# Optimization experiments

Hardware: AMD Instinct MI355X
Metric: run time of the kernel (lower is better)

The kernel has to match this reference:

```python
import jax, jax.numpy as jnp
import numpy as np

F = 16      # frames
NV = 4096   # visual points per frame
NT = 512    # tactile points per frame
M = 4096    # model points
SCALE = 0.1


def setup_inputs() -> dict:
    key = jax.random.key(0)
    ks = jax.random.split(key, 6)
    return {
        "state": jax.random.normal(ks[0], (6,), dtype=jnp.float32) * 0.1,
        "model_points": jax.random.normal(ks[1], (M, 3), dtype=jnp.float32),
        "visual_points": jax.random.normal(ks[2], (F, NV, 3), dtype=jnp.float32),
        "tactile_points": jax.random.normal(ks[3], (F, NT, 3), dtype=jnp.float32),
        "physics_pred_states": jax.random.normal(ks[4], (F, 12), dtype=jnp.float32) * 0.1,
        "delta_time": jax.random.uniform(ks[5], (F,), dtype=jnp.float32, minval=0.01, maxval=0.05),
    }


def _skew(a):
    z = jnp.zeros((), a.dtype)
    return jnp.array([[z, -a[2], a[1]],
                      [a[2], z, -a[0]],
                      [-a[1], a[0], z]])


def _rot_from_omega(omega, dt):
    # Rodrigues: R = I + sin(theta*dt) S + (1 - cos(theta*dt)) S@S, S = skew(omega/|omega|)
    theta = jnp.linalg.norm(omega)
    ax = omega / jnp.clip(theta, 1e-8)
    S = _skew(ax)
    return jnp.eye(3, dtype=omega.dtype) + jnp.sin(theta * dt) * S + (1.0 - jnp.cos(theta * dt)) * (S @ S)


def _chamfer(pred, gt):
    # rows: pred [N,3], cols: gt [M,3]; row-min of squared distances, then mean
    d = (jnp.sum(pred * pred, axis=1)[:, None]
         + jnp.sum(gt * gt, axis=1)[None, :]
         - 2.0 * pred @ gt.T)
    return jnp.mean(jnp.min(d, axis=1))


def reference(state, model_points, visual_points, tactile_points, physics_pred_states, delta_time):
    t0 = state[:3]
    r0 = _rot_from_omega(state[3:], jnp.float32(1.0))  # Euler2Mat modeled as axis-angle

    def pose_step(carry, x):
        t, r = carry
        v, omega, dt = x
        t = t + v * dt
        r = _rot_from_omega(omega, dt) @ r
        return (t, r), (t, r)

    _, (ts, rs) = jax.lax.scan(
        pose_step, (t0, r0),
        (physics_pred_states[1:, 6:9], physics_pred_states[1:, 9:12], delta_time[1:]))
    ts = jnp.concatenate([t0[None], ts], axis=0)  # [F,3]
    rs = jnp.concatenate([r0[None], rs], axis=0)  # [F,3,3]

    def frame_loss(acc, x):
        t, r, vp, tp = x
        vc = ((vp - t) @ r) / SCALE
        tc = ((tp - t) @ r) / SCALE
        acc = acc + _chamfer(vc, model_points) + 0.1 * _chamfer(tc, model_points)
        return acc, None

    E_cd, _ = jax.lax.scan(frame_loss, jnp.zeros((), jnp.float32),
                           (ts, rs, visual_points, tactile_points))
    return E_cd
```

## Files before the change

### kernel.cpp

```cpp
#include <hip/hip_runtime.h>
#include <math.h>

#define F_    16
#define NV_   4096
#define NT_   512
#define M_    4096
#define PPF_  (NV_ + NT_)
#define NPTS_ (F_ * PPF_)
#define SCALE_INV 10.0f

#define TPB    256
#define PPT    8
#define PPB    (TPB * PPT)
#define NPB    (NPTS_ / PPB)
#define CHUNK  128
#define NCHUNK (M_ / CHUNK)

__device__ inline void rot_from_omega(float ox, float oy, float oz, float dt,
                                      float* R) {
    float theta = sqrtf(ox * ox + oy * oy + oz * oz);
    float inv = 1.0f / fmaxf(theta, 1e-8f);
    float ax = ox * inv, ay = oy * inv, az = oz * inv;
    float s = sinf(theta * dt);
    float c = 1.0f - cosf(theta * dt);
    R[0] = 1.0f - c * (ay * ay + az * az);
    R[1] = -s * az + c * ax * ay;
    R[2] =  s * ay + c * ax * az;
    R[3] =  s * az + c * ax * ay;
    R[4] = 1.0f - c * (ax * ax + az * az);
    R[5] = -s * ax + c * ay * az;
    R[6] = -s * ax * 0.0f + c * 0.0f;
    R[6] = -s * ay + c * ax * az;
    R[7] =  s * ax + c * ay * az;
    R[8] = 1.0f - c * (ax * ax + ay * ay);
}

__global__ void pose_kernel(const float* __restrict__ state,
                            const float* __restrict__ phys,
                            const float* __restrict__ dts,
                            float* __restrict__ poses,
                            float* __restrict__ out) {
    __shared__ float sRs[F_ * 9];
    __shared__ float sdt[F_ * 3];
    int f = threadIdx.x;
    if (f == 0) out[0] = 0.0f;
    if (f >= 1 && f < F_) {
        float Rs[9];
        float dt = dts[f];
        rot_from_omega(phys[f * 12 + 9], phys[f * 12 + 10], phys[f * 12 + 11], dt, Rs);
        for (int j = 0; j < 9; ++j) sRs[f * 9 + j] = Rs[j];
        sdt[f * 3 + 0] = phys[f * 12 + 6] * dt;
        sdt[f * 3 + 1] = phys[f * 12 + 7] * dt;
        sdt[f * 3 + 2] = phys[f * 12 + 8] * dt;
    }
    __syncthreads();
    if (f == 0) {
        float t[3] = {state[0], state[1], state[2]};
        float R[9];
        rot_from_omega(state[3], state[4], state[5], 1.0f, R);
        for (int i = 0; i < F_; ++i) {
            if (i > 0) {
                t[0] += sdt[i * 3 + 0];
                t[1] += sdt[i * 3 + 1];
                t[2] += sdt[i * 3 + 2];
                float Rn[9];
                const float* Rs = sRs + i * 9;
                for (int r = 0; r < 3; ++r)
                    for (int c2 = 0; c2 < 3; ++c2)
                        Rn[r * 3 + c2] = Rs[r * 3 + 0] * R[0 + c2] +
                                         Rs[r * 3 + 1] * R[3 + c2] +
                                         Rs[r * 3 + 2] * R[6 + c2];
                for (int j = 0; j < 9; ++j) R[j] = Rn[j];
            }
            float* o = poses + i * 12;
            o[0] = t[0]; o[1] = t[1]; o[2] = t[2];
            for (int j = 0; j < 9; ++j) o[3 + j] = R[j] * SCALE_INV;
        }
    }
}

__global__ __launch_bounds__(TPB) void chamfer_main(
    const float* __restrict__ model, const float* __restrict__ vis,
    const float* __restrict__ tac, const float* __restrict__ poses,
    float* __restrict__ partials) {
    __shared__ float4 sfeat[CHUNK];
    __shared__ float sposes[F_ * 12];
    const int pb = blockIdx.x;
    const int ch = blockIdx.y;
    const int mbase = ch * CHUNK;

    if (threadIdx.x < F_ * 12) sposes[threadIdx.x] = poses[threadIdx.x];

    if (threadIdx.x < CHUNK) {
        int i = threadIdx.x;
        float gx = model[(mbase + i) * 3 + 0];
        float gy = model[(mbase + i) * 3 + 1];
        float gz = model[(mbase + i) * 3 + 2];
        sfeat[i] = make_float4(-2.0f * gx, -2.0f * gy, -2.0f * gz,
                               gx * gx + gy * gy + gz * gz);
    }
    __syncthreads();

    float c0[PPT], c1[PPT], c2[PPT], cn[PPT], dm[PPT];
#pragma unroll
    for (int k = 0; k < PPT; ++k) {
        int pt = pb * PPB + k * TPB + threadIdx.x;
        int f = pt / PPF_;
        int loc = pt - f * PPF_;
        const float* p = (loc < NV_) ? (vis + ((size_t)f * NV_ + loc) * 3)
                                     : (tac + ((size_t)f * NT_ + (loc - NV_)) * 3);
        float px = p[0], py = p[1], pz = p[2];
        const float* ps = sposes + f * 12;
        float d0 = px - ps[0], d1 = py - ps[1], d2 = pz - ps[2];
        const float* R = ps + 3;
        float x = d0 * R[0] + d1 * R[3] + d2 * R[6];
        float y = d0 * R[1] + d1 * R[4] + d2 * R[7];
        float z = d0 * R[2] + d1 * R[5] + d2 * R[8];
        c0[k] = x; c1[k] = y; c2[k] = z;
        cn[k] = x * x + y * y + z * z;
        dm[k] = 3.4e38f;
    }

#pragma unroll 4
    for (int m = 0; m < CHUNK; m += 2) {
        float4 ga = sfeat[m];
        float4 gb = sfeat[m + 1];
#pragma unroll
        for (int k = 0; k < PPT; ++k) {
            float da = fmaf(ga.x, c0[k], fmaf(ga.y, c1[k], fmaf(ga.z, c2[k], ga.w)));
            float db = fmaf(gb.x, c0[k], fmaf(gb.y, c1[k], fmaf(gb.z, c2[k], gb.w)));
            dm[k] = fminf(dm[k], fminf(da, db));
        }
    }

#pragma unroll
    for (int k = 0; k < PPT; ++k) {
        int pt = pb * PPB + k * TPB + threadIdx.x;
        partials[(size_t)ch * NPTS_ + pt] = dm[k] + cn[k];
    }
}

__global__ __launch_bounds__(TPB) void chamfer_reduce(
    const float* __restrict__ partials, float* __restrict__ out) {
    int pt = blockIdx.x * TPB + threadIdx.x;
    float m = partials[pt];
    for (int ch = 1; ch < NCHUNK; ++ch)
        m = fminf(m, partials[(size_t)ch * NPTS_ + pt]);
    int loc = pt % PPF_;
    float w = (loc < NV_) ? (1.0f / NV_) : (0.1f / NT_);
    float v = m * w;
#pragma unroll
    for (int off = 32; off > 0; off >>= 1) v += __shfl_down(v, off);
    __shared__ float sw[TPB / 64];
    if ((threadIdx.x & 63) == 0) sw[threadIdx.x >> 6] = v;
    __syncthreads();
    if (threadIdx.x == 0) {
        float s = 0.0f;
        for (int i = 0; i < TPB / 64; ++i) s += sw[i];
        atomicAdd(out, s);
    }
}

#define FB_PPT  2
#define FB_PPB  (TPB * FB_PPT)
#define FB_NPB  (NPTS_ / FB_PPB)

__device__ inline void compute_pose_serial(int f, const float* state,
                                           const float* phys, const float* dts,
                                           float* t, float* R) {
    t[0] = state[0]; t[1] = state[1]; t[2] = state[2];
    rot_from_omega(state[3], state[4], state[5], 1.0f, R);
    for (int i = 1; i <= f; ++i) {
        float dt = dts[i];
        t[0] += phys[i * 12 + 6] * dt;
        t[1] += phys[i * 12 + 7] * dt;
        t[2] += phys[i * 12 + 8] * dt;
        float Rs[9];
        rot_from_omega(phys[i * 12 + 9], phys[i * 12 + 10], phys[i * 12 + 11], dt, Rs);
        float Rn[9];
        for (int r = 0; r < 3; ++r)
            for (int c2 = 0; c2 < 3; ++c2)
                Rn[r * 3 + c2] = Rs[r * 3 + 0] * R[0 + c2] +
                                 Rs[r * 3 + 1] * R[3 + c2] +
                                 Rs[r * 3 + 2] * R[6 + c2];
        for (int j = 0; j < 9; ++j) R[j] = Rn[j];
    }
}

__global__ __launch_bounds__(TPB) void chamfer_fused(
    const float* __restrict__ state, const float* __restrict__ model,
    const float* __restrict__ vis, const float* __restrict__ tac,
    const float* __restrict__ phys, const float* __restrict__ dts,
    float* __restrict__ out) {
    __shared__ float4 sfeat[CHUNK];
    __shared__ float sposes[F_ * 12];
    __shared__ float sw[TPB / 64];

    if (threadIdx.x < F_) {
        float t[3], R[9];
        compute_pose_serial(threadIdx.x, state, phys, dts, t, R);
        float* o = sposes + threadIdx.x * 12;
        o[0] = t[0]; o[1] = t[1]; o[2] = t[2];
        for (int j = 0; j < 9; ++j) o[3 + j] = R[j] * SCALE_INV;
    }
    __syncthreads();

    float c0[FB_PPT], c1[FB_PPT], c2[FB_PPT], cn[FB_PPT], dm[FB_PPT], wt[FB_PPT];
#pragma unroll
    for (int k = 0; k < FB_PPT; ++k) {
        int pt = blockIdx.x * FB_PPB + k * TPB + threadIdx.x;
        int f = pt / PPF_;
        int loc = pt - f * PPF_;
        wt[k] = (loc < NV_) ? (1.0f / NV_) : (0.1f / NT_);
        const float* p = (loc < NV_) ? (vis + ((size_t)f * NV_ + loc) * 3)
                                     : (tac + ((size_t)f * NT_ + (loc - NV_)) * 3);
        float px = p[0], py = p[1], pz = p[2];
        const float* ps = sposes + f * 12;
        float d0 = px - ps[0], d1 = py - ps[1], d2 = pz - ps[2];
        const float* R = ps + 3;
        float x = d0 * R[0] + d1 * R[3] + d2 * R[6];
        float y = d0 * R[1] + d1 * R[4] + d2 * R[7];
        float z = d0 * R[2] + d1 * R[5] + d2 * R[8];
        c0[k] = x; c1[k] = y; c2[k] = z;
        cn[k] = x * x + y * y + z * z;
        dm[k] = 3.4e38f;
    }

    for (int ch = 0; ch < NCHUNK; ++ch) {
        __syncthreads();
        if (threadIdx.x < CHUNK) {
            int i = threadIdx.x;
            int mi = ch * CHUNK + i;
            float gx = model[mi * 3 + 0], gy = model[mi * 3 + 1], gz = model[mi * 3 + 2];
            sfeat[i] = make_float4(-2.0f * gx, -2.0f * gy, -2.0f * gz,
                                   gx * gx + gy * gy + gz * gz);
        }
        __syncthreads();
#pragma unroll 4
        for (int m = 0; m < CHUNK; m += 2) {
            float4 ga = sfeat[m];
            float4 gb = sfeat[m + 1];
#pragma unroll
            for (int k = 0; k < FB_PPT; ++k) {
                float da = fmaf(ga.x, c0[k], fmaf(ga.y, c1[k], fmaf(ga.z, c2[k], ga.w)));
                float db = fmaf(gb.x, c0[k], fmaf(gb.y, c1[k], fmaf(gb.z, c2[k], gb.w)));
                dm[k] = fminf(dm[k], fminf(da, db));
            }
        }
    }

    float v = 0.0f;
#pragma unroll
    for (int k = 0; k < FB_PPT; ++k) v += (dm[k] + cn[k]) * wt[k];
#pragma unroll
    for (int off = 32; off > 0; off >>= 1) v += __shfl_down(v, off);
    if ((threadIdx.x & 63) == 0) sw[threadIdx.x >> 6] = v;
    __syncthreads();
    if (threadIdx.x == 0) {
        float s = 0.0f;
        for (int i = 0; i < TPB / 64; ++i) s += sw[i];
        atomicAdd(out, s);
    }
}

extern "C" void kernel_launch(void* const* d_in, const int* in_sizes, int n_in,
                              void* d_out, int out_size, void* d_ws, size_t ws_size,
                              hipStream_t stream) {
    const float* state = (const float*)d_in[0];
    const float* model = (const float*)d_in[1];
    const float* vis   = (const float*)d_in[2];
    const float* tac   = (const float*)d_in[3];
    const float* phys  = (const float*)d_in[4];
    const float* dts   = (const float*)d_in[5];
    float* out = (float*)d_out;

    const size_t partial_bytes = (size_t)NCHUNK * NPTS_ * sizeof(float);
    const size_t need = partial_bytes + F_ * 12 * sizeof(float);

    if (ws_size >= need) {
        float* partials = (float*)d_ws;
        float* poses = (float*)((char*)d_ws + partial_bytes);
        pose_kernel<<<1, 64, 0, stream>>>(state, phys, dts, poses, out);
        dim3 grid(NPB, NCHUNK);
        chamfer_main<<<grid, TPB, 0, stream>>>(model, vis, tac, poses, partials);
        chamfer_reduce<<<NPTS_ / TPB, TPB, 0, stream>>>(partials, out);
    } else {
        hipMemsetAsync(out, 0, sizeof(float), stream);
        chamfer_fused<<<FB_NPB, TPB, 0, stream>>>(state, model, vis, tac, phys, dts,
                                                  out);
    }
}
```

Before: 104.1 us.

## Fuse chamfer into single kernel with split-M reduction in shared memory

Replaces the three-kernel path (pose kernel, chamfer partials over model chunks, min-reduce) with one kernel. Each block owns 64 query points from a single frame. Threads split the model points 32 ways and keep a double-buffered shared-memory tile of model features, using rotated indexing to reduce bank conflicts. The per-split minima are reduced in shared memory, which removes the large global partials buffer and its write and read traffic. In exchange, every block recomputes the poses serially and the 4-way-duplicated model loads and per-chunk barriers add overhead.

```diff
diff --git a/kernel.cpp b/kernel.cpp
--- a/kernel.cpp
+++ b/kernel.cpp
@@ -9,12 +9,14 @@
 #define NPTS_ (F_ * PPF_)
 #define SCALE_INV 10.0f
 
-#define TPB    256
-#define PPT    8
-#define PPB    (TPB * PPT)
-#define NPB    (NPTS_ / PPB)
-#define CHUNK  128
-#define NCHUNK (M_ / CHUNK)
+#define TPB     256
+#define PTSB    64
+#define NBLK    (NPTS_ / PTSB)
+#define CHUNK   128
+#define NCHUNK  (M_ / CHUNK)
+#define NSPLIT  32
+#define MPS     (CHUNK / NSPLIT)
+#define PPT     8
 
 __device__ inline void rot_from_omega(float ox, float oy, float oz, float dt,
                                       float* R) {
@@ -29,141 +31,10 @@
     R[3] =  s * az + c * ax * ay;
     R[4] = 1.0f - c * (ax * ax + az * az);
     R[5] = -s * ax + c * ay * az;
-    R[6] = -s * ax * 0.0f + c * 0.0f;
     R[6] = -s * ay + c * ax * az;
     R[7] =  s * ax + c * ay * az;
     R[8] = 1.0f - c * (ax * ax + ay * ay);
 }
-
-__global__ void pose_kernel(const float* __restrict__ state,
-                            const float* __restrict__ phys,
-                            const float* __restrict__ dts,
-                            float* __restrict__ poses,
-                            float* __restrict__ out) {
-    __shared__ float sRs[F_ * 9];
-    __shared__ float sdt[F_ * 3];
-    int f = threadIdx.x;
-    if (f == 0) out[0] = 0.0f;
-    if (f >= 1 && f < F_) {
-        float Rs[9];
-        float dt = dts[f];
-        rot_from_omega(phys[f * 12 + 9], phys[f * 12 + 10], phys[f * 12 + 11], dt, Rs);
-        for (int j = 0; j < 9; ++j) sRs[f * 9 + j] = Rs[j];
-        sdt[f * 3 + 0] = phys[f * 12 + 6] * dt;
-        sdt[f * 3 + 1] = phys[f * 12 + 7] * dt;
-        sdt[f * 3 + 2] = phys[f * 12 + 8] * dt;
-    }
-    __syncthreads();
-    if (f == 0) {
-        float t[3] = {state[0], state[1], state[2]};
-        float R[9];
-        rot_from_omega(state[3], state[4], state[5], 1.0f, R);
-        for (int i = 0; i < F_; ++i) {
-            if (i > 0) {
-                t[0] += sdt[i * 3 + 0];
-                t[1] += sdt[i * 3 + 1];
-                t[2] += sdt[i * 3 + 2];
-                float Rn[9];
-                const float* Rs = sRs + i * 9;
-                for (int r = 0; r < 3; ++r)
-                    for (int c2 = 0; c2 < 3; ++c2)
-                        Rn[r * 3 + c2] = Rs[r * 3 + 0] * R[0 + c2] +
-                                         Rs[r * 3 + 1] * R[3 + c2] +
-                                         Rs[r * 3 + 2] * R[6 + c2];
-                for (int j = 0; j < 9; ++j) R[j] = Rn[j];
-            }
-            float* o = poses + i * 12;
-            o[0] = t[0]; o[1] = t[1]; o[2] = t[2];
-            for (int j = 0; j < 9; ++j) o[3 + j] = R[j] * SCALE_INV;
-        }
-    }
-}
-
-__global__ __launch_bounds__(TPB) void chamfer_main(
-    const float* __restrict__ model, const float* __restrict__ vis,
-    const float* __restrict__ tac, const float* __restrict__ poses,
-    float* __restrict__ partials) {
-    __shared__ float4 sfeat[CHUNK];
-    __shared__ float sposes[F_ * 12];
-    const int pb = blockIdx.x;
-    const int ch = blockIdx.y;
-    const int mbase = ch * CHUNK;
-
-    if (threadIdx.x < F_ * 12) sposes[threadIdx.x] = poses[threadIdx.x];
-
-    if (threadIdx.x < CHUNK) {
-        int i = threadIdx.x;
-        float gx = model[(mbase + i) * 3 + 0];
-        float gy = model[(mbase + i) * 3 + 1];
-        float gz = model[(mbase + i) * 3 + 2];
-        sfeat[i] = make_float4(-2.0f * gx, -2.0f * gy, -2.0f * gz,
-                               gx * gx + gy * gy + gz * gz);
-    }
-    __syncthreads();
-
-    float c0[PPT], c1[PPT], c2[PPT], cn[PPT], dm[PPT];
-#pragma unroll
-    for (int k = 0; k < PPT; ++k) {
-        int pt = pb * PPB + k * TPB + threadIdx.x;
-        int f = pt / PPF_;
-        int loc = pt - f * PPF_;
-        const float* p = (loc < NV_) ? (vis + ((size_t)f * NV_ + loc) * 3)
-                                     : (tac + ((size_t)f * NT_ + (loc - NV_)) * 3);
-        float px = p[0], py = p[1], pz = p[2];
-        const float* ps = sposes + f * 12;
-        float d0 = px - ps[0], d1 = py - ps[1], d2 = pz - ps[2];
-        const float* R = ps + 3;
-        float x = d0 * R[0] + d1 * R[3] + d2 * R[6];
-        float y = d0 * R[1] + d1 * R[4] + d2 * R[7];
-        float z = d0 * R[2] + d1 * R[5] + d2 * R[8];
-        c0[k] = x; c1[k] = y; c2[k] = z;
-        cn[k] = x * x + y * y + z * z;
-        dm[k] = 3.4e38f;
-    }
-
-#pragma unroll 4
-    for (int m = 0; m < CHUNK; m += 2) {
-        float4 ga = sfeat[m];
-        float4 gb = sfeat[m + 1];
-#pragma unroll
-        for (int k = 0; k < PPT; ++k) {
-            float da = fmaf(ga.x, c0[k], fmaf(ga.y, c1[k], fmaf(ga.z, c2[k], ga.w)));
-            float db = fmaf(gb.x, c0[k], fmaf(gb.y, c1[k], fmaf(gb.z, c2[k], gb.w)));
-            dm[k] = fminf(dm[k], fminf(da, db));
-        }
-    }
-
-#pragma unroll
-    for (int k = 0; k < PPT; ++k) {
-        int pt = pb * PPB + k * TPB + threadIdx.x;
-        partials[(size_t)ch * NPTS_ + pt] = dm[k] + cn[k];
-    }
-}
-
-__global__ __launch_bounds__(TPB) void chamfer_reduce(
-    const float* __restrict__ partials, float* __restrict__ out) {
-    int pt = blockIdx.x * TPB + threadIdx.x;
-    float m = partials[pt];
-    for (int ch = 1; ch < NCHUNK; ++ch)
-        m = fminf(m, partials[(size_t)ch * NPTS_ + pt]);
-    int loc = pt % PPF_;
-    float w = (loc < NV_) ? (1.0f / NV_) : (0.1f / NT_);
-    float v = m * w;
-#pragma unroll
-    for (int off = 32; off > 0; off >>= 1) v += __shfl_down(v, off);
-    __shared__ float sw[TPB / 64];
-    if ((threadIdx.x & 63) == 0) sw[threadIdx.x >> 6] = v;
-    __syncthreads();
-    if (threadIdx.x == 0) {
-        float s = 0.0f;
-        for (int i = 0; i < TPB / 64; ++i) s += sw[i];
-        atomicAdd(out, s);
-    }
-}
-
-#define FB_PPT  2
-#define FB_PPB  (TPB * FB_PPT)
-#define FB_NPB  (NPTS_ / FB_PPB)
 
 __device__ inline void compute_pose_serial(int f, const float* state,
                                            const float* phys, const float* dts,
@@ -187,31 +58,43 @@
     }
 }
 
-__global__ __launch_bounds__(TPB) void chamfer_fused(
+__global__ __launch_bounds__(TPB) void chamfer_one(
     const float* __restrict__ state, const float* __restrict__ model,
     const float* __restrict__ vis, const float* __restrict__ tac,
     const float* __restrict__ phys, const float* __restrict__ dts,
     float* __restrict__ out) {
-    __shared__ float4 sfeat[CHUNK];
-    __shared__ float sposes[F_ * 12];
-    __shared__ float sw[TPB / 64];
+    __shared__ float4 featD[2][TPB];
+    __shared__ float  sposes[F_ * 12];
+    __shared__ float  sdm[PTSB][NSPLIT + 1];
 
-    if (threadIdx.x < F_) {
-        float t[3], R[9];
-        compute_pose_serial(threadIdx.x, state, phys, dts, t, R);
-        float* o = sposes + threadIdx.x * 12;
-        o[0] = t[0]; o[1] = t[1]; o[2] = t[2];
+    const int t = threadIdx.x;
+
+    if (t < F_) {
+        float tr[3], R[9];
+        compute_pose_serial(t, state, phys, dts, tr, R);
+        float* o = sposes + t * 12;
+        o[0] = tr[0]; o[1] = tr[1]; o[2] = tr[2];
         for (int j = 0; j < 9; ++j) o[3 + j] = R[j] * SCALE_INV;
+    }
+
+    {
+        const int mi = (t >> 3) * MPS + (t & 3);
+        float gx = model[mi * 3 + 0], gy = model[mi * 3 + 1], gz = model[mi * 3 + 2];
+        featD[0][t] = make_float4(-2.0f * gx, -2.0f * gy, -2.0f * gz,
+                                  gx * gx + gy * gy + gz * gz);
     }
     __syncthreads();
 
-    float c0[FB_PPT], c1[FB_PPT], c2[FB_PPT], cn[FB_PPT], dm[FB_PPT], wt[FB_PPT];
+    const int pg  = t & 7;
+    const int sp  = t >> 3;
+    const int rot = t & 3;
+    const int f   = (blockIdx.x * PTSB) / PPF_;
+    const int lbase = blockIdx.x * PTSB - f * PPF_;
+
+    float c0[PPT], c1[PPT], c2[PPT], cn[PPT], dm[PPT];
 #pragma unroll
-    for (int k = 0; k < FB_PPT; ++k) {
-        int pt = blockIdx.x * FB_PPB + k * TPB + threadIdx.x;
-        int f = pt / PPF_;
-        int loc = pt - f * PPF_;
-        wt[k] = (loc < NV_) ? (1.0f / NV_) : (0.1f / NT_);
+    for (int k = 0; k < PPT; ++k) {
+        int loc = lbase + pg * PPT + k;
         const float* p = (loc < NV_) ? (vis + ((size_t)f * NV_ + loc) * 3)
                                      : (tac + ((size_t)f * NT_ + (loc - NV_)) * 3);
         float px = p[0], py = p[1], pz = p[2];
@@ -226,40 +109,43 @@
         dm[k] = 3.4e38f;
     }
 
-    for (int ch = 0; ch < NCHUNK; ++ch) {
-        __syncthreads();
-        if (threadIdx.x < CHUNK) {
-            int i = threadIdx.x;
-            int mi = ch * CHUNK + i;
+    for (int c = 0; c < NCHUNK; ++c) {
+        const int cur = c & 1;
+        if (c + 1 < NCHUNK) {
+            const int mi = (c + 1) * CHUNK + sp * MPS + (t & 3);
             float gx = model[mi * 3 + 0], gy = model[mi * 3 + 1], gz = model[mi * 3 + 2];
-            sfeat[i] = make_float4(-2.0f * gx, -2.0f * gy, -2.0f * gz,
-                                   gx * gx + gy * gy + gz * gz);
+            featD[cur ^ 1][t] = make_float4(-2.0f * gx, -2.0f * gy, -2.0f * gz,
+                                            gx * gx + gy * gy + gz * gz);
         }
-        __syncthreads();
-#pragma unroll 4
-        for (int m = 0; m < CHUNK; m += 2) {
-            float4 ga = sfeat[m];
-            float4 gb = sfeat[m + 1];
+        const float4* fb = &featD[cur][sp * 8];
 #pragma unroll
-            for (int k = 0; k < FB_PPT; ++k) {
+        for (int m = 0; m < MPS; m += 2) {
+            float4 ga = fb[rot + m];
+            float4 gb = fb[rot + m + 1];
+#pragma unroll
+            for (int k = 0; k < PPT; ++k) {
                 float da = fmaf(ga.x, c0[k], fmaf(ga.y, c1[k], fmaf(ga.z, c2[k], ga.w)));
                 float db = fmaf(gb.x, c0[k], fmaf(gb.y, c1[k], fmaf(gb.z, c2[k], gb.w)));
                 dm[k] = fminf(dm[k], fminf(da, db));
             }
         }
+        __syncthreads();
     }
 
-    float v = 0.0f;
 #pragma unroll
-    for (int k = 0; k < FB_PPT; ++k) v += (dm[k] + cn[k]) * wt[k];
+    for (int k = 0; k < PPT; ++k) sdm[pg * PPT + k][sp] = dm[k] + cn[k];
+    __syncthreads();
+
+    if (t < PTSB) {
+        float mn = sdm[t][0];
 #pragma unroll
-    for (int off = 32; off > 0; off >>= 1) v += __shfl_down(v, off);
-    if ((threadIdx.x & 63) == 0) sw[threadIdx.x >> 6] = v;
-    __syncthreads();
-    if (threadIdx.x == 0) {
-        float s = 0.0f;
-        for (int i = 0; i < TPB / 64; ++i) s += sw[i];
-        atomicAdd(out, s);
+        for (int i = 1; i < NSPLIT; ++i) mn = fminf(mn, sdm[t][i]);
+        const int loc = lbase + t;
+        const float w = (loc < NV_) ? (1.0f / NV_) : (0.1f / NT_);
+        float v = mn * w;
+#pragma unroll
+        for (int off = 32; off > 0; off >>= 1) v += __shfl_down(v, off);
+        if (t == 0) atomicAdd(out, v);
     }
 }
 
@@ -273,20 +159,8 @@
     const float* phys  = (const float*)d_in[4];
     const float* dts   = (const float*)d_in[5];
     float* out = (float*)d_out;
+    (void)d_ws; (void)ws_size;
 
-    const size_t partial_bytes = (size_t)NCHUNK * NPTS_ * sizeof(float);
-    const size_t need = partial_bytes + F_ * 12 * sizeof(float);
-
-    if (ws_size >= need) {
-        float* partials = (float*)d_ws;
-        float* poses = (float*)((char*)d_ws + partial_bytes);
-        pose_kernel<<<1, 64, 0, stream>>>(state, phys, dts, poses, out);
-        dim3 grid(NPB, NCHUNK);
-        chamfer_main<<<grid, TPB, 0, stream>>>(model, vis, tac, poses, partials);
-        chamfer_reduce<<<NPTS_ / TPB, TPB, 0, stream>>>(partials, out);
-    } else {
-        hipMemsetAsync(out, 0, sizeof(float), stream);
-        chamfer_fused<<<FB_NPB, TPB, 0, stream>>>(state, model, vis, tac, phys, dts,
-                                                  out);
-    }
+    hipMemsetAsync(out, 0, sizeof(float), stream);
+    chamfer_one<<<NBLK, TPB, 0, stream>>>(state, model, vis, tac, phys, dts, out);
 }
```

New measurement: 113.0 us. 8.5% more time.
